# Optimization experiments

Hardware: AMD Instinct MI355X
Metric: run time of the kernel (lower is better)

Reference implementation:

```python
import jax, jax.numpy as jnp
import numpy as np

B, DIM, HEADS, H, W = 2, 256, 8, 40, 40


def setup_inputs() -> dict:
    key = jax.random.key(0)
    ks = jax.random.split(key, 11)
    s = 0.05
    return {
        "x": jax.random.normal(ks[0], (B, DIM, H, W), jnp.float32),
        "qkv_w": jax.random.normal(ks[1], (3 * DIM, DIM, 1, 1), jnp.float32) * s,
        "qkv_b": jax.random.normal(ks[2], (3 * DIM,), jnp.float32) * s,
        "pos_w": jax.random.normal(ks[3], (3 * DIM, 1, 3, 3), jnp.float32) * s,
        "pos_b": jax.random.normal(ks[4], (3 * DIM,), jnp.float32) * s,
        "proj_w": jax.random.normal(ks[5], (DIM, DIM), jnp.float32) * s,
        "proj_b": jax.random.normal(ks[6], (DIM,), jnp.float32) * s,
        "g1_w": jax.random.normal(ks[7], (16, 1), jnp.float32),
        "g1_b": jax.random.normal(ks[8], (16,), jnp.float32),
        "g2_w": jax.random.normal(ks[9], (1, 16), jnp.float32),
        "g2_b": jax.random.normal(ks[10], (1,), jnp.float32),
    }


def _conv(x, w, b, groups=1, pad=0):
    # NCHW conv, OIHW weights (matches torch Conv2d)
    y = jax.lax.conv_general_dilated(x, w, (1, 1), [(pad, pad), (pad, pad)],
                                     feature_group_count=groups)
    return y + b[None, :, None, None]


def reference(x, qkv_w, qkv_b, pos_w, pos_b, proj_w, proj_b, g1_w, g1_b, g2_w, g2_b):
    b, c, h, w = x.shape
    n = h * w
    hd = c // HEADS
    scale = hd ** -0.5

    qkv = _conv(x, qkv_w, qkv_b)                     # [b, 3c, h, w]
    qkv = _conv(qkv, pos_w, pos_b, groups=3 * c, pad=1)  # depthwise 3x3
    q, k, v = jnp.split(qkv, 3, axis=1)

    def to_heads(t):  # [b,c,h,w] -> [b, heads, n, head_dim]
        return t.reshape(b, HEADS, hd, n).transpose(0, 1, 3, 2)

    q, k, v = to_heads(q), to_heads(k), to_heads(v)

    attn = jnp.einsum('bhnd,bhmd->bhnm', q, k) * scale      # [b,H,n,n]
    prob = jax.nn.softmax(attn, axis=-1)
    entropy = -(prob * jnp.log(jnp.clip(prob, 1e-12))).sum(-1).mean(-1)  # [b,H]

    # EntropyGate: ratio in [0.1, 1.0]
    hid = jax.nn.relu(entropy[..., None] @ g1_w.T + g1_b)
    ratio = jax.nn.sigmoid(hid @ g2_w.T + g2_b)[..., 0] * 0.9 + 0.1      # [b,H]

    # dynamic per-(b,head) top-k: keep = ceil(ratio*n), clamped to [1,n]
    keep = jnp.clip(jnp.ceil(ratio * n).astype(jnp.int32), 1, n)          # [b,H]
    srt = jnp.flip(jnp.sort(attn, axis=-1), axis=-1)                      # descending
    idx = jnp.broadcast_to((keep - 1)[:, :, None, None], (b, HEADS, n, 1))
    kth = jnp.take_along_axis(srt, idx, axis=-1)                          # [b,H,n,1]
    sparse = jnp.where(attn >= kth, attn, -jnp.inf)

    p = jax.nn.softmax(sparse, axis=-1)
    out = jnp.einsum('bhnm,bhmd->bhnd', p, v)
    out = out.transpose(0, 2, 1, 3).reshape(b, n, c)
    out = out @ proj_w.T + proj_b
    return out.transpose(0, 2, 1).reshape(b, c, h, w)
```

## Files before the change

### kernel.cpp

```cpp
#include <hip/hip_runtime.h>
#include <math.h>

#define BB 2
#define CDIM 256
#define NHEADS 8
#define HD 32
#define HH 40
#define WW 40
#define NN 1600
#define C3 768
#define SCALE 0.17677669529663687f
#define RTE 8
#define RTS 2
#define TSTR 2048
#define HSTR 51200

__device__ inline unsigned fkey(float f) {
    unsigned u = __float_as_uint(f);
    return (u & 0x80000000u) ? ~u : (u | 0x80000000u);
}
__device__ inline float finv(unsigned u) {
    unsigned v = (u & 0x80000000u) ? (u ^ 0x80000000u) : ~u;
    return __uint_as_float(v);
}

__global__ __launch_bounds__(256) void conv1x1_kernel(const float* __restrict__ x,
                                                      const float* __restrict__ w,
                                                      const float* __restrict__ bias,
                                                      float* __restrict__ out) {
    int blk = blockIdx.x;
    int st = blk % 7;
    int t2 = blk / 7;
    int ocg = t2 % (C3 / 8);
    int b = t2 / (C3 / 8);
    int s = st * 256 + threadIdx.x;
    if (s >= NN) return;
    int oc0 = ocg * 8;
    const float* xb = x + (size_t)b * CDIM * NN + s;
    const float* w0 = w + (size_t)oc0 * CDIM;
    float a[8];
#pragma unroll
    for (int i = 0; i < 8; i++) a[i] = bias[oc0 + i];
#pragma unroll 4
    for (int ic = 0; ic < CDIM; ic++) {
        float xv = xb[(size_t)ic * NN];
#pragma unroll
        for (int i = 0; i < 8; i++) a[i] += w0[i * CDIM + ic] * xv;
    }
    float* ob = out + ((size_t)b * C3 + oc0) * NN + s;
#pragma unroll
    for (int i = 0; i < 8; i++) ob[(size_t)i * NN] = a[i];
}

__global__ __launch_bounds__(256) void dwconv_kernel(const float* __restrict__ in,
                                                     const float* __restrict__ w,
                                                     const float* __restrict__ bias,
                                                     float* __restrict__ out_t) {
    int idx = blockIdx.x * 256 + threadIdx.x;
    int s = idx % NN;
    int t = idx / NN;
    int c = t % C3;
    int b = t / C3;
    int y = s / WW, xx = s % WW;
    const float* ib = in + ((size_t)b * C3 + c) * NN;
    const float* wr = w + (size_t)c * 9;
    float acc = bias[c];
#pragma unroll
    for (int ky = 0; ky < 3; ky++) {
        int iy = y + ky - 1;
        if (iy < 0 || iy >= HH) continue;
#pragma unroll
        for (int kx = 0; kx < 3; kx++) {
            int ix = xx + kx - 1;
            if (ix < 0 || ix >= WW) continue;
            acc += wr[ky * 3 + kx] * ib[iy * WW + ix];
        }
    }
    int part = c >> 8;
    int r = c & 255;
    int hh = r >> 5;
    int d = r & 31;
    out_t[((size_t)(b * 3 + part) * NHEADS + hh) * HSTR + (s >> 6) * TSTR + d * 64 + (s & 63)] = acc;
}

template <int PERSIST>
__global__ __launch_bounds__(256) void entropy_kernel(const float* __restrict__ qkv_t,
                                                      float* __restrict__ ent,
                                                      float* __restrict__ attw) {
    int blk = blockIdx.x;
    int rt = blk % (NN / RTE);
    int bh = blk / (NN / RTE);
    int h = bh % NHEADS, b = bh / NHEADS;
    int row0 = rt * RTE;
    __shared__ float Qs[RTE][HD];
    int tid = threadIdx.x;
    const float* qt = qkv_t + ((size_t)(b * 3 + 0) * NHEADS + h) * HSTR;
    const float* ktb = qkv_t + ((size_t)(b * 3 + 1) * NHEADS + h) * HSTR;
    {
        int r = tid >> 5, d = tid & 31;
        int row = row0 + r;
        Qs[r][d] = qt[(row >> 6) * TSTR + d * 64 + (row & 63)];
    }
    __syncthreads();
    int w = tid >> 6, lane = tid & 63;
    int lr0 = 2 * w, lr1 = lr0 + 1;
    float* aw0 = nullptr;
    float* aw1 = nullptr;
    if (PERSIST) {
        aw0 = attw + ((size_t)bh * NN + row0 + lr0) * NN;
        aw1 = aw0 + NN;
    }
    float q0[HD], q1[HD];
#pragma unroll
    for (int d = 0; d < HD; d++) { q0[d] = Qs[lr0][d]; q1[d] = Qs[lr1][d]; }
    float S0 = 0.f, T0 = 0.f, S1 = 0.f, T1 = 0.f;
#pragma unroll 1
    for (int kt = 0; kt < 25; kt++) {
        const float* kp = ktb + kt * TSTR + lane;
        float a0 = 0.f, a1 = 0.f;
#pragma unroll
        for (int dc = 0; dc < 4; dc++) {
            float kc[8];
#pragma unroll
            for (int i = 0; i < 8; i++) kc[i] = kp[(dc * 8 + i) * 64];
#pragma unroll
            for (int i = 0; i < 8; i++) {
                a0 += q0[dc * 8 + i] * kc[i];
                a1 += q1[dc * 8 + i] * kc[i];
            }
        }
        a0 *= SCALE; a1 *= SCALE;
        if (PERSIST) {
            int j = kt * 64 + lane;
            aw0[j] = a0;
            aw1[j] = a1;
        }
        float e0 = __expf(a0), e1 = __expf(a1);
        S0 += e0; T0 += e0 * a0;
        S1 += e1; T1 += e1 * a1;
    }
#pragma unroll
    for (int o = 1; o < 64; o <<= 1) {
        S0 += __shfl_xor(S0, o); T0 += __shfl_xor(T0, o);
        S1 += __shfl_xor(S1, o); T1 += __shfl_xor(T1, o);
    }
    if (lane == 0) {
        ent[(size_t)bh * NN + row0 + lr0] = logf(S0) - T0 / S0;
        ent[(size_t)bh * NN + row0 + lr1] = logf(S1) - T1 / S1;
    }
}

__global__ void gate_kernel(const float* __restrict__ ent_rows,
                            const float* __restrict__ g1w, const float* __restrict__ g1b,
                            const float* __restrict__ g2w, const float* __restrict__ g2b,
                            int* __restrict__ keep) {
    int bh = blockIdx.x;
    int tid = threadIdx.x;
    __shared__ float red[4];
    float ls = 0.f;
    for (int j = tid; j < NN; j += 256) ls += ent_rows[bh * NN + j];
    for (int o = 32; o > 0; o >>= 1) ls += __shfl_down(ls, o);
    int lane = tid & 63, wid = tid >> 6;
    if (lane == 0) red[wid] = ls;
    __syncthreads();
    if (tid == 0) {
        float ent = (red[0] + red[1] + red[2] + red[3]) / (float)NN;
        float val = g2b[0];
#pragma unroll
        for (int j = 0; j < 16; j++) {
            float hid = ent * g1w[j] + g1b[j];
            if (hid < 0.f) hid = 0.f;
            val += hid * g2w[j];
        }
        float ratio = 0.9f / (1.f + expf(-val)) + 0.1f;
        int kp = (int)ceilf(ratio * (float)NN);
        if (kp < 1) kp = 1;
        if (kp > NN) kp = NN;
        keep[bh] = kp;
    }
}

__global__ __launch_bounds__(256, 4) void select_kernel(const float* __restrict__ attbuf,
                                                        const int* __restrict__ keep,
                                                        float* __restrict__ kth_out,
                                                        float* __restrict__ m_out) {
    int blk = blockIdx.x;
    int rt = blk % (NN / 8);
    int bh = blk / (NN / 8);
    int row0 = rt * 8;
    __shared__ unsigned hist[4][RTS][256];
    int tid = threadIdx.x;
    int wv = tid >> 6;
    int lane = tid & 63;
    int wrow0 = row0 + 2 * wv;
    int want = keep[bh];
    int l = lane & 31;
    int r = (lane < 32) ? 0 : 1;
    const float* ar = attbuf + ((size_t)bh * NN + wrow0 + r) * NN;

    unsigned kvr[50];
#pragma unroll
    for (int k2 = 0; k2 < 50; k2++) kvr[k2] = fkey(ar[k2 * 32 + l]);

    unsigned mk = 0u;
#pragma unroll
    for (int k2 = 0; k2 < 50; k2++) mk = mk > kvr[k2] ? mk : kvr[k2];
#pragma unroll
    for (int off = 1; off < 32; off <<= 1) {
        unsigned o = (unsigned)__shfl_xor((int)mk, off);
        mk = mk > o ? mk : o;
    }

    unsigned prefixHigh = 0;
    for (int pass = 0; pass < 4; pass++) {
        int shift = 24 - 8 * pass;
#pragma unroll
        for (int i = 0; i < 8; i++) hist[wv][r][248 - 8 * l + i] = 0u;
#pragma unroll
        for (int k2 = 0; k2 < 50; k2++) {
            unsigned u = kvr[k2];
            bool ok = (pass == 0) || ((u >> (shift + 8)) == prefixHigh);
            if (ok) atomicAdd(&hist[wv][r][(u >> shift) & 255u], 1u);
        }
        unsigned sch = 0;
#pragma unroll
        for (int i = 0; i < 8; i++) sch += hist[wv][r][248 - 8 * l + i];
        unsigned inc = sch;
#pragma unroll
        for (int dlt = 1; dlt < 32; dlt <<= 1) {
            unsigned tv = __shfl_up(inc, dlt, 32);
            if (l >= dlt) inc += tv;
        }
        unsigned pref = inc - sch;
        bool found = (pref < (unsigned)want) && ((unsigned)want <= inc);
        int bsel = -1, wnew = 0;
        if (found) {
            unsigned want2 = (unsigned)want - pref, cum = 0;
#pragma unroll
            for (int i = 0; i < 8; i++) {
                int bbin = 255 - 8 * l - i;
                unsigned c = hist[wv][r][bbin];
                if (bsel < 0 && cum + c >= want2) { bsel = bbin; wnew = (int)(want2 - cum); }
                cum += c;
            }
        }
        unsigned long long mkb = __ballot(found);
        int src = (lane < 32) ? __builtin_ctzll(mkb & 0xffffffffULL)
                              : __builtin_ctzll(mkb >> 32) + 32;
        bsel = __shfl(bsel, src);
        want = __shfl(wnew, src);
        prefixHigh = (prefixHigh << 8) | (unsigned)bsel;
    }
    if (l == 0) {
        kth_out[(size_t)bh * NN + wrow0 + r] = finv(prefixHigh);
        m_out[(size_t)bh * NN + wrow0 + r] = finv(mk);
    }
}

__global__ __launch_bounds__(256, 4) void pv_kernel(const float* __restrict__ qkv_t,
                                                    const float* __restrict__ attbuf,
                                                    const float* __restrict__ kth_in,
                                                    const float* __restrict__ m_in,
                                                    float* __restrict__ oht) {
    int blk = blockIdx.x;
    int rt = blk % (NN / 8);
    int bh = blk / (NN / 8);
    int h = bh % NHEADS, b = bh / NHEADS;
    int row0 = rt * 8;
    __shared__ float scratch[4][64 * 33];
    int tid = threadIdx.x;
    int wv = tid >> 6;
    int lane = tid & 63;
    int r0 = row0 + 2 * wv;
    const float* vtb = qkv_t + ((size_t)(b * 3 + 2) * NHEADS + h) * HSTR;
    const float* ab0 = attbuf + ((size_t)bh * NN + r0) * NN;
    const float* ab1 = ab0 + NN;
    float m0 = m_in[(size_t)bh * NN + r0];
    float m1 = m_in[(size_t)bh * NN + r0 + 1];
    float kth0 = kth_in[(size_t)bh * NN + r0];
    float kth1 = kth_in[(size_t)bh * NN + r0 + 1];

    float acc0[HD], acc1[HD];
#pragma unroll
    for (int d = 0; d < HD; d++) { acc0[d] = 0.f; acc1[d] = 0.f; }
    float S0 = 0.f, S1 = 0.f;
    for (int kt = 0; kt < 25; kt++) {
        const float* vp = vtb + kt * TSTR + lane;
        int j = kt * 64 + lane;
        float a0 = ab0[j];
        float a1 = ab1[j];
        float p0 = (a0 >= kth0) ? __expf(a0 - m0) : 0.f;
        float p1 = (a1 >= kth1) ? __expf(a1 - m1) : 0.f;
        S0 += p0; S1 += p1;
#pragma unroll
        for (int d = 0; d < HD; d++) {
            float vv = vp[d * 64];
            acc0[d] += p0 * vv;
            acc1[d] += p1 * vv;
        }
    }
#pragma unroll
    for (int off = 1; off < 64; off <<= 1) {
        S0 += __shfl_xor(S0, off);
        S1 += __shfl_xor(S1, off);
    }

    float* sc = &scratch[wv][0];
    int dd = lane & 31;
    int jb = (lane < 32) ? 0 : 32;
#pragma unroll
    for (int d = 0; d < HD; d++) sc[lane * 33 + d] = acc0[d];
    float sum0 = 0.f;
#pragma unroll
    for (int jj = 0; jj < 32; jj++) sum0 += sc[(jb + jj) * 33 + dd];
    sum0 += __shfl_xor(sum0, 32);
#pragma unroll
    for (int d = 0; d < HD; d++) sc[lane * 33 + d] = acc1[d];
    float sum1 = 0.f;
#pragma unroll
    for (int jj = 0; jj < 32; jj++) sum1 += sc[(jb + jj) * 33 + dd];
    sum1 += __shfl_xor(sum1, 32);

    if (lane < 32) {
        size_t base = ((size_t)b * CDIM + h * HD + dd) * NN + r0;
        oht[base + 0] = sum0 / S0;
        oht[base + 1] = sum1 / S1;
    }
}

__global__ __launch_bounds__(64) void sparse_attn_kernel(const float* __restrict__ qkv_t,
                                                         const int* __restrict__ keep,
                                                         float* __restrict__ oht) {
    int blk = blockIdx.x;
    int rt = blk % (NN / RTS);
    int bh = blk / (NN / RTS);
    int h = bh % NHEADS, b = bh / NHEADS;
    int row0 = rt * RTS;
    __shared__ float att[RTS][NN];
    __shared__ unsigned hist[RTS][256];
    __shared__ float Qs[RTS][HD];
    int tid = threadIdx.x;
    const float* qt = qkv_t + ((size_t)(b * 3 + 0) * NHEADS + h) * HSTR;
    const float* ktb = qkv_t + ((size_t)(b * 3 + 1) * NHEADS + h) * HSTR;
    const float* vtb = qkv_t + ((size_t)(b * 3 + 2) * NHEADS + h) * HSTR;
    {
        int r = tid >> 5, d = tid & 31;
        int row = row0 + r;
        Qs[r][d] = qt[(row >> 6) * TSTR + d * 64 + (row & 63)];
    }
    int want = keep[bh];
    __syncthreads();
    int lane = tid;
    float q0[HD], q1[HD];
#pragma unroll
    for (int d = 0; d < HD; d++) { q0[d] = Qs[0][d]; q1[d] = Qs[1][d]; }
    float m0 = -1e30f, m1 = -1e30f;
    for (int kt = 0; kt < 25; kt++) {
        const float* kp = ktb + kt * TSTR + lane;
        int j = kt * 64 + lane;
        float kc[HD];
#pragma unroll
        for (int d = 0; d < HD; d++) kc[d] = kp[d * 64];
        float a0 = 0.f, a1 = 0.f;
#pragma unroll
        for (int d = 0; d < HD; d++) { a0 += q0[d] * kc[d]; a1 += q1[d] * kc[d]; }
        a0 *= SCALE; a1 *= SCALE;
        att[0][j] = a0;
        att[1][j] = a1;
        m0 = fmaxf(m0, a0); m1 = fmaxf(m1, a1);
    }
#pragma unroll
    for (int off = 1; off < 64; off <<= 1) {
        m0 = fmaxf(m0, __shfl_xor(m0, off));
        m1 = fmaxf(m1, __shfl_xor(m1, off));
    }
    int l = lane & 31;
    int r = (lane < 32) ? 0 : 1;
    unsigned kvr[50];
#pragma unroll
    for (int k2 = 0; k2 < 50; k2++) kvr[k2] = fkey(att[r][k2 * 32 + l]);
    unsigned prefixHigh = 0;
    for (int pass = 0; pass < 4; pass++) {
        int shift = 24 - 8 * pass;
#pragma unroll
        for (int i = 0; i < 8; i++) hist[r][248 - 8 * l + i] = 0u;
#pragma unroll
        for (int k2 = 0; k2 < 50; k2++) {
            unsigned u = kvr[k2];
            bool ok = (pass == 0) || ((u >> (shift + 8)) == prefixHigh);
            if (ok) atomicAdd(&hist[r][(u >> shift) & 255u], 1u);
        }
        unsigned sch = 0;
#pragma unroll
        for (int i = 0; i < 8; i++) sch += hist[r][248 - 8 * l + i];
        unsigned inc = sch;
#pragma unroll
        for (int dlt = 1; dlt < 32; dlt <<= 1) {
            unsigned tv = __shfl_up(inc, dlt, 32);
            if (l >= dlt) inc += tv;
        }
        unsigned pref = inc - sch;
        bool found = (pref < (unsigned)want) && ((unsigned)want <= inc);
        int bsel = -1, wnew = 0;
        if (found) {
            unsigned want2 = (unsigned)want - pref, cum = 0;
#pragma unroll
            for (int i = 0; i < 8; i++) {
                int bbin = 255 - 8 * l - i;
                unsigned c = hist[r][bbin];
                if (bsel < 0 && cum + c >= want2) { bsel = bbin; wnew = (int)(want2 - cum); }
                cum += c;
            }
        }
        unsigned long long mk = __ballot(found);
        int src = (lane < 32) ? __builtin_ctzll(mk & 0xffffffffULL)
                              : __builtin_ctzll(mk >> 32) + 32;
        bsel = __shfl(bsel, src);
        want = __shfl(wnew, src);
        prefixHigh = (prefixHigh << 8) | (unsigned)bsel;
    }
    float kth = finv(prefixHigh);
    float kth0 = __shfl(kth, 0);
    float kth1 = __shfl(kth, 32);
    float acc0[HD], acc1[HD];
#pragma unroll
    for (int d = 0; d < HD; d++) { acc0[d] = 0.f; acc1[d] = 0.f; }
    float S0 = 0.f, S1 = 0.f;
    for (int kt = 0; kt < 25; kt++) {
        const float* vp = vtb + kt * TSTR + lane;
        int j = kt * 64 + lane;
        float a0 = att[0][j];
        float a1 = att[1][j];
        float p0 = (a0 >= kth0) ? __expf(a0 - m0) : 0.f;
        float p1 = (a1 >= kth1) ? __expf(a1 - m1) : 0.f;
        S0 += p0; S1 += p1;
#pragma unroll
        for (int d = 0; d < HD; d++) {
            float vv = vp[d * 64];
            acc0[d] += p0 * vv;
            acc1[d] += p1 * vv;
        }
    }
#pragma unroll
    for (int off = 1; off < 64; off <<= 1) {
        S0 += __shfl_xor(S0, off);
        S1 += __shfl_xor(S1, off);
    }
    float* scratch = &att[0][0];
    int dd = lane & 31;
    int jb = (lane < 32) ? 0 : 32;
#pragma unroll
    for (int d = 0; d < HD; d++) scratch[lane * 33 + d] = acc0[d];
    float sum0 = 0.f;
#pragma unroll
    for (int jj = 0; jj < 32; jj++) sum0 += scratch[(jb + jj) * 33 + dd];
    sum0 += __shfl_xor(sum0, 32);
#pragma unroll
    for (int d = 0; d < HD; d++) scratch[lane * 33 + d] = acc1[d];
    float sum1 = 0.f;
#pragma unroll
    for (int jj = 0; jj < 32; jj++) sum1 += scratch[(jb + jj) * 33 + dd];
    sum1 += __shfl_xor(sum1, 32);
    if (lane < 32) {
        size_t base = ((size_t)b * CDIM + h * HD + dd) * NN + row0;
        oht[base + 0] = sum0 / S0;
        oht[base + 1] = sum1 / S1;
    }
}

__global__ __launch_bounds__(256) void proj_kernel(const float* __restrict__ oht,
                                                   const float* __restrict__ pw,
                                                   const float* __restrict__ pb,
                                                   float* __restrict__ out) {
    int blk = blockIdx.x;
    int st = blk % 7;
    int t2 = blk / 7;
    int ocg = t2 % (CDIM / 8);
    int b = t2 / (CDIM / 8);
    int s = st * 256 + threadIdx.x;
    if (s >= NN) return;
    int co0 = ocg * 8;
    const float* ib = oht + (size_t)b * CDIM * NN + s;
    const float* w0 = pw + (size_t)co0 * CDIM;
    float a[8];
#pragma unroll
    for (int i = 0; i < 8; i++) a[i] = pb[co0 + i];
#pragma unroll 4
    for (int c = 0; c < CDIM; c++) {
        float xv = ib[(size_t)c * NN];
#pragma unroll
        for (int i = 0; i < 8; i++) a[i] += w0[i * CDIM + c] * xv;
    }
    float* ob = out + ((size_t)b * CDIM + co0) * NN + s;
#pragma unroll
    for (int i = 0; i < 8; i++) ob[(size_t)i * NN] = a[i];
}

extern "C" void kernel_launch(void* const* d_in, const int* in_sizes, int n_in,
                              void* d_out, int out_size, void* d_ws, size_t ws_size,
                              hipStream_t stream) {
    const float* x      = (const float*)d_in[0];
    const float* qkv_w  = (const float*)d_in[1];
    const float* qkv_b  = (const float*)d_in[2];
    const float* pos_w  = (const float*)d_in[3];
    const float* pos_b  = (const float*)d_in[4];
    const float* proj_w = (const float*)d_in[5];
    const float* proj_b = (const float*)d_in[6];
    const float* g1w    = (const float*)d_in[7];
    const float* g1b    = (const float*)d_in[8];
    const float* g2w    = (const float*)d_in[9];
    const float* g2b    = (const float*)d_in[10];
    float* out = (float*)d_out;

    float* ws   = (float*)d_ws;
    float* buf1 = ws;
    float* buf2 = buf1 + (size_t)BB * C3 * NN;
    float* ent  = buf2 + (size_t)BB * C3 * NN;
    float* oht  = ent + (size_t)BB * NHEADS * NN;
    int* keep   = (int*)(oht + (size_t)BB * CDIM * NN);
    float* kth  = (float*)(keep + 16);
    float* mrow = kth + (size_t)BB * NHEADS * NN;
    float* attbuf = mrow + (size_t)BB * NHEADS * NN;
    size_t need = (size_t)((char*)(attbuf + (size_t)BB * NHEADS * NN * NN) - (char*)d_ws);
    bool persist = (ws_size >= need);

    conv1x1_kernel<<<BB * (C3 / 8) * 7, 256, 0, stream>>>(x, qkv_w, qkv_b, buf1);
    dwconv_kernel<<<BB * C3 * NN / 256, 256, 0, stream>>>(buf1, pos_w, pos_b, buf2);
    if (persist) {
        entropy_kernel<1><<<NHEADS * BB * (NN / RTE), 256, 0, stream>>>(buf2, ent, attbuf);
        gate_kernel<<<BB * NHEADS, 256, 0, stream>>>(ent, g1w, g1b, g2w, g2b, keep);
        select_kernel<<<NHEADS * BB * (NN / 8), 256, 0, stream>>>(attbuf, keep, kth, mrow);
        pv_kernel<<<NHEADS * BB * (NN / 8), 256, 0, stream>>>(buf2, attbuf, kth, mrow, oht);
    } else {
        entropy_kernel<0><<<NHEADS * BB * (NN / RTE), 256, 0, stream>>>(buf2, ent, nullptr);
        gate_kernel<<<BB * NHEADS, 256, 0, stream>>>(ent, g1w, g1b, g2w, g2b, keep);
        sparse_attn_kernel<<<NHEADS * BB * (NN / RTS), 64, 0, stream>>>(buf2, keep, oht);
    }
    proj_kernel<<<BB * (CDIM / 8) * 7, 256, 0, stream>>>(oht, proj_w, proj_b, out);
}
```

Baseline: 419.7 us.

## Stage V tiles through double-buffered LDS in pv_kernel with register prefetch

In pv_kernel, each V tile (32x64 floats) used to be read from global memory by all four waves separately. It is now loaded once per block with float4 loads into a double-buffered LDS area, and the next tile is prefetched into registers while the current one is consumed. The final reduction now folds the two half-waves with shuffles before the LDS transpose-sum, which halves the LDS writes. The cost is a __syncthreads per tile and extra LDS traffic. There is also a possible race: the LDS reduction area overlaps buffer 0 while other waves may still be reading it, although a barrier is placed before it.

Measured after the change: 414.1 us. Within noise of the previous version (-1.3%).

```diff
diff --git a/kernel.cpp b/kernel.cpp
--- a/kernel.cpp
+++ b/kernel.cpp
@@ -14,6 +14,8 @@
 #define RTS 2
 #define TSTR 2048
 #define HSTR 51200
+
+typedef __attribute__((ext_vector_type(4))) float f4;
 
 __device__ inline unsigned fkey(float f) {
     unsigned u = __float_as_uint(f);
@@ -267,7 +269,7 @@
     int bh = blk / (NN / 8);
     int h = bh % NHEADS, b = bh / NHEADS;
     int row0 = rt * 8;
-    __shared__ float scratch[4][64 * 33];
+    __shared__ float lds[4224];
     int tid = threadIdx.x;
     int wv = tid >> 6;
     int lane = tid & 63;
@@ -284,8 +286,28 @@
 #pragma unroll
     for (int d = 0; d < HD; d++) { acc0[d] = 0.f; acc1[d] = 0.f; }
     float S0 = 0.f, S1 = 0.f;
+
+    f4 st0, st1;
+    {
+        const f4* vp = (const f4*)vtb;
+        st0 = vp[tid];
+        st1 = vp[256 + tid];
+    }
+    int cur = 0;
+#pragma unroll 1
     for (int kt = 0; kt < 25; kt++) {
-        const float* vp = vtb + kt * TSTR + lane;
+        {
+            f4* dst = (f4*)&lds[cur * 2048];
+            dst[tid] = st0;
+            dst[256 + tid] = st1;
+        }
+        __syncthreads();
+        if (kt + 1 < 25) {
+            const f4* vp = (const f4*)(vtb + (kt + 1) * TSTR);
+            st0 = vp[tid];
+            st1 = vp[256 + tid];
+        }
+        const float* vb = &lds[cur * 2048];
         int j = kt * 64 + lane;
         float a0 = ab0[j];
         float a1 = ab1[j];
@@ -294,10 +316,11 @@
         S0 += p0; S1 += p1;
 #pragma unroll
         for (int d = 0; d < HD; d++) {
-            float vv = vp[d * 64];
+            float vv = vb[d * 64 + lane];
             acc0[d] += p0 * vv;
             acc1[d] += p1 * vv;
         }
+        cur ^= 1;
     }
 #pragma unroll
     for (int off = 1; off < 64; off <<= 1) {
@@ -305,21 +328,28 @@
         S1 += __shfl_xor(S1, off);
     }
 
-    float* sc = &scratch[wv][0];
+#pragma unroll
+    for (int d = 0; d < HD; d++) {
+        acc0[d] += __shfl_xor(acc0[d], 32);
+        acc1[d] += __shfl_xor(acc1[d], 32);
+    }
+    __syncthreads();
+    float* sc = &lds[wv * 1056];
     int dd = lane & 31;
-    int jb = (lane < 32) ? 0 : 32;
-#pragma unroll
-    for (int d = 0; d < HD; d++) sc[lane * 33 + d] = acc0[d];
+    if (lane < 32) {
+#pragma unroll
+        for (int d = 0; d < HD; d++) sc[lane * 33 + d] = acc0[d];
+    }
     float sum0 = 0.f;
 #pragma unroll
-    for (int jj = 0; jj < 32; jj++) sum0 += sc[(jb + jj) * 33 + dd];
-    sum0 += __shfl_xor(sum0, 32);
-#pragma unroll
-    for (int d = 0; d < HD; d++) sc[lane * 33 + d] = acc1[d];
+    for (int jj = 0; jj < 32; jj++) sum0 += sc[jj * 33 + dd];
+    if (lane < 32) {
+#pragma unroll
+        for (int d = 0; d < HD; d++) sc[lane * 33 + d] = acc1[d];
+    }
     float sum1 = 0.f;
 #pragma unroll
-    for (int jj = 0; jj < 32; jj++) sum1 += sc[(jb + jj) * 33 + dd];
-    sum1 += __shfl_xor(sum1, 32);
+    for (int jj = 0; jj < 32; jj++) sum1 += sc[jj * 33 + dd];
 
     if (lane < 32) {
         size_t base = ((size_t)b * CDIM + h * HD + dd) * NN + r0;
```
